# Kernel tuning notes

Measured on AMD Instinct MI355X. Metric: run time of the kernel, lower is better.

Reference implementation:

```python
import jax, jax.numpy as jnp
import numpy as np

H = 64        # index_n_heads
D = 128       # index_head_dim
R = 64        # rope_head_dim
TOPK = 512    # index_topk
FP8_MAX = 448.0
EPS = 1e-6
THETA = 10000.0


def setup_inputs() -> dict:
    key = jax.random.key(0)
    ks = jax.random.split(key, 6)
    T, DM, QL = 1536, 7168, 1536
    return {
        "hidden_states": jax.random.normal(ks[0], (T, DM), jnp.float32),
        "q_lora": jax.random.normal(ks[1], (T, QL), jnp.float32),
        "wq_b": jax.random.normal(ks[2], (QL, H * D), jnp.float32) / np.sqrt(QL),
        "wk": jax.random.normal(ks[3], (DM, D), jnp.float32) / np.sqrt(DM),
        "k_norm_w": jnp.ones((D,), jnp.float32),
        "k_norm_b": jnp.zeros((D,), jnp.float32),
        "weights_proj_w": jax.random.normal(ks[4], (DM, H), jnp.float32) / np.sqrt(DM),
        "positions": jnp.arange(T, dtype=jnp.int32),
    }


def _rope_neox(x, pos):
    # x: [T, ..., R]; pos: [T]. NEOX-style (half-split) rotary on the rope slice.
    half = R // 2
    inv = 1.0 / (THETA ** (jnp.arange(half, dtype=jnp.float32) / half))
    ang = pos.astype(jnp.float32)[:, None] * inv  # [T, half]
    cos, sin = jnp.cos(ang), jnp.sin(ang)
    while cos.ndim < x.ndim:
        cos, sin = cos[:, None, :], sin[:, None, :]
    x1, x2 = x[..., :half], x[..., half:]
    return jnp.concatenate([x1 * cos - x2 * sin, x2 * cos + x1 * sin], axis=-1)


def _fp8_quant(x):
    # per-row (last-dim) e4m3 quantization: value -> fp8 payload + fp32 scale
    scale = jnp.maximum(jnp.max(jnp.abs(x), axis=-1, keepdims=True) / FP8_MAX, 1e-12)
    xq = (x / scale).astype(jnp.float8_e4m3fn).astype(jnp.float32)
    return xq, scale


def reference(hidden_states, q_lora, wq_b, wk, k_norm_w, k_norm_b, weights_proj_w, positions):
    T = hidden_states.shape[0]
    softmax_scale = D ** (-0.5)
    weights_scale = H ** (-0.5)

    # projections
    q = (q_lora @ wq_b).reshape(T, H, D)          # wq_b
    k = hidden_states @ wk                        # wk

    # k_norm (LayerNorm)
    mu = jnp.mean(k, axis=-1, keepdims=True)
    var = jnp.mean((k - mu) ** 2, axis=-1, keepdims=True)
    k = (k - mu) * jax.lax.rsqrt(var + EPS) * k_norm_w + k_norm_b

    # RoPE on the first rope_head_dim dims of q and k
    q = jnp.concatenate([_rope_neox(q[..., :R], positions), q[..., R:]], axis=-1)
    k = jnp.concatenate([_rope_neox(k[..., :R], positions), k[..., R:]], axis=-1)

    # fp8 quantization (per token-head for q, per token for k)
    q_fp8, q_scale = _fp8_quant(q)   # [T,H,D], [T,H,1]
    k_fp8, k_scale = _fp8_quant(k)   # [T,D],   [T,1]

    # head-gate weights: weights_proj(x) * q_scale * softmax_scale * weights_scale
    gate = hidden_states @ weights_proj_w                      # [T,H]
    w = gate[..., None] * q_scale * (softmax_scale * weights_scale)  # [T,H,1]

    # index score: I[t,s] = sum_h w[t,h] * relu(q[t,h] . k[s]) * k_scale[s]
    qk = jnp.einsum('thd,sd->ths', q_fp8, k_fp8)               # [T,H,S]
    score = jnp.einsum('th,ths->ts', w[..., 0], jax.nn.relu(qk))
    score = score * k_scale[:, 0][None, :]

    # causal (ragged prefill) mask + topk block selection
    causal = positions[:, None] >= positions[None, :]
    score = jnp.where(causal, score, -jnp.inf)
    vals, idx = jax.lax.top_k(score, TOPK)
    idx = jnp.where(jnp.isfinite(vals), idx, -1)
    return idx, vals
```

## Files before the change

kernel.cpp:

```cpp
#include <hip/hip_runtime.h>
#include <hip/hip_bf16.h>
#include <math.h>

#define T_SZ 1536
#define DM_SZ 7168
#define QL_SZ 1536
#define H_SZ 64
#define D_SZ 128
#define ND 8192
#define TOPK_SZ 512
#define N2 192
#define SPLITK2 16

typedef float f32x4 __attribute__((ext_vector_type(4)));
typedef short s16x8 __attribute__((ext_vector_type(8)));
typedef unsigned long long u64;

static __device__ __forceinline__ unsigned char f32_to_e4m3(float x){
  unsigned int b = __float_as_uint(x);
  unsigned int s = (b >> 24) & 0x80u;
  float a = fabsf(x);
  if (a < 0.015625f){
    int m = (int)rintf(a * 512.0f);
    if (m == 8) return (unsigned char)(s | 0x08u);
    return (unsigned char)(s | (unsigned)m);
  }
  int e;
  float mant = frexpf(a, &e);
  int E = e - 1;
  int m = (int)rintf(mant * 16.0f) - 8;
  if (m == 8){ E += 1; m = 0; }
  if (E > 8 || (E == 8 && m > 6)) return (unsigned char)(s | 0x7Eu);
  return (unsigned char)(s | ((unsigned)(E + 7) << 3) | (unsigned)m);
}

static __device__ __forceinline__ unsigned short bf16_rne(float x){
  unsigned int u = __float_as_uint(x);
  return (unsigned short)((u + 0x7FFFu + ((u >> 16) & 1u)) >> 16);
}

typedef __attribute__((address_space(1))) const void gas_void;
typedef __attribute__((address_space(3))) void las_void;
static __device__ __forceinline__ void stage16(const void* g, void* l){
  __builtin_amdgcn_global_load_lds((gas_void*)g, (las_void*)l, 16, 0, 0);
}

__global__ void rope_table_k(const int* __restrict__ pos, float* __restrict__ cs){
  int i = blockIdx.x * blockDim.x + threadIdx.x;
  if (i >= T_SZ * 32) return;
  int t = i >> 5, j = i & 31;
  float inv = 1.0f / powf(10000.0f, (float)j * (1.0f / 32.0f));
  float ang = (float)pos[t] * inv;
  cs[t * 64 + j]      = cosf(ang);
  cs[t * 64 + 32 + j] = sinf(ang);
}

__global__ __launch_bounds__(256) void conv_split_k(const float* __restrict__ A,
                                                    unsigned short* __restrict__ hi,
                                                    unsigned short* __restrict__ lo,
                                                    int n4){
  int i = blockIdx.x * 256 + threadIdx.x;
  if (i >= n4) return;
  float4 v = *(const float4*)&A[(size_t)i * 4];
  float f[4] = {v.x, v.y, v.z, v.w};
  unsigned short hb[4], lb[4];
#pragma unroll
  for (int j = 0; j < 4; ++j){
    hb[j] = bf16_rne(f[j]);
    float hf = __uint_as_float((unsigned int)hb[j] << 16);
    lb[j] = bf16_rne(f[j] - hf);
  }
  ushort4 h, l;
  h.x = hb[0]; h.y = hb[1]; h.z = hb[2]; h.w = hb[3];
  l.x = lb[0]; l.y = lb[1]; l.z = lb[2]; l.w = lb[3];
  *(ushort4*)&hi[(size_t)i * 4] = h;
  *(ushort4*)&lo[(size_t)i * 4] = l;
}

__global__ __launch_bounds__(256) void convB_k(const float* __restrict__ B,
                                               unsigned short* __restrict__ bhi,
                                               unsigned short* __restrict__ blo){
  __shared__ float ld[32][33];
  const int n0 = blockIdx.x * 32, k0 = blockIdx.y * 32;
  const int t = threadIdx.x;
  const int r = t >> 3, c4 = (t & 7) * 4;
  float4 v = *(const float4*)&B[(size_t)(k0 + r) * ND + n0 + c4];
  ld[r][c4 + 0] = v.x; ld[r][c4 + 1] = v.y; ld[r][c4 + 2] = v.z; ld[r][c4 + 3] = v.w;
  __syncthreads();
  unsigned short hb[4], lb[4];
#pragma unroll
  for (int j = 0; j < 4; ++j){
    float x = ld[c4 + j][r];
    hb[j] = bf16_rne(x);
    float hf = __uint_as_float((unsigned int)hb[j] << 16);
    lb[j] = bf16_rne(x - hf);
  }
  ushort4 h, l;
  h.x = hb[0]; h.y = hb[1]; h.z = hb[2]; h.w = hb[3];
  l.x = lb[0]; l.y = lb[1]; l.z = lb[2]; l.w = lb[3];
  *(ushort4*)&bhi[(size_t)(n0 + r) * QL_SZ + k0 + c4] = h;
  *(ushort4*)&blo[(size_t)(n0 + r) * QL_SZ + k0 + c4] = l;
}

__global__ __launch_bounds__(256) void conv_w2_k(const float* __restrict__ wk,
                                                 const float* __restrict__ wp,
                                                 unsigned short* __restrict__ bhi,
                                                 unsigned short* __restrict__ blo){
  __shared__ float ld[32][33];
  const int n0 = blockIdx.x * 32, k0 = blockIdx.y * 32;
  const int t = threadIdx.x;
  const int r = t >> 3, c4 = (t & 7) * 4;
  float4 v;
  if (n0 < 128) v = *(const float4*)&wk[(size_t)(k0 + r) * 128 + n0 + c4];
  else          v = *(const float4*)&wp[(size_t)(k0 + r) * 64 + (n0 - 128) + c4];
  ld[r][c4 + 0] = v.x; ld[r][c4 + 1] = v.y; ld[r][c4 + 2] = v.z; ld[r][c4 + 3] = v.w;
  __syncthreads();
  unsigned short hb[4], lb[4];
#pragma unroll
  for (int j = 0; j < 4; ++j){
    float x = ld[c4 + j][r];
    hb[j] = bf16_rne(x);
    float hf = __uint_as_float((unsigned int)hb[j] << 16);
    lb[j] = bf16_rne(x - hf);
  }
  ushort4 h, l;
  h.x = hb[0]; h.y = hb[1]; h.z = hb[2]; h.w = hb[3];
  l.x = lb[0]; l.y = lb[1]; l.z = lb[2]; l.w = lb[3];
  *(ushort4*)&bhi[(size_t)(n0 + r) * DM_SZ + k0 + c4] = h;
  *(ushort4*)&blo[(size_t)(n0 + r) * DM_SZ + k0 + c4] = l;
}

__global__ __launch_bounds__(256) void gemm1_mfma_k(const unsigned short* __restrict__ Ahi,
                                                    const unsigned short* __restrict__ Alo,
                                                    const unsigned short* __restrict__ Bhi,
                                                    const unsigned short* __restrict__ Blo,
                                                    float* __restrict__ C){
  __shared__ unsigned short As [128 * 64];
  __shared__ unsigned short Bs0[128 * 64];
  __shared__ unsigned short Bs1[128 * 64];
  const int bid = blockIdx.x;
  const int lid = (bid & 7) * 96 + (bid >> 3);
  const int mt = lid % 12, nt = lid / 12;
  const int m0 = mt * 128, n0 = nt * 128;
  const int tid = threadIdx.x;
  const int w = tid >> 6, l = tid & 63;
  const int wr = w >> 1, wc = w & 1;
  const int lr = l & 15, lg = l >> 4;

  const int srow = w * 32 + (l >> 3);
  const int ssl  = (l & 7) ^ ((l >> 3) & 7);
  const size_t gA = (size_t)(m0 + srow) * QL_SZ + ssl * 8;
  const size_t gB = (size_t)(n0 + srow) * QL_SZ + ssl * 8;
  const int lbase = w * 2048;

  f32x4 acc[4][4];
#pragma unroll
  for (int i = 0; i < 4; ++i)
#pragma unroll
    for (int j = 0; j < 4; ++j) acc[i][j] = (f32x4){0.f, 0.f, 0.f, 0.f};

  const int amrow = wr * 64 + lr;
  const int bnrow = wc * 64 + lr;

  for (int k0 = 0; k0 < QL_SZ; k0 += 64){
#pragma unroll
    for (int i = 0; i < 4; ++i){
      size_t go = (size_t)i * 8 * QL_SZ + k0;
      stage16(Ahi + gA + go, As  + lbase + i * 512);
      stage16(Bhi + gB + go, Bs0 + lbase + i * 512);
      stage16(Blo + gB + go, Bs1 + lbase + i * 512);
    }
    __syncthreads();
#pragma unroll
    for (int kk = 0; kk < 2; ++kk){
      s16x8 af[4], b0[4], b1[4];
#pragma unroll
      for (int f = 0; f < 4; ++f){
        int ma = amrow + f * 16;
        int nb = bnrow + f * 16;
        int sa = ((kk * 4 + lg) ^ (ma & 7)) * 16;
        int sb = ((kk * 4 + lg) ^ (nb & 7)) * 16;
        af[f] = *(const s16x8*)((const char*)As  + ma * 128 + sa);
        b0[f] = *(const s16x8*)((const char*)Bs0 + nb * 128 + sb);
        b1[f] = *(const s16x8*)((const char*)Bs1 + nb * 128 + sb);
      }
#pragma unroll
      for (int fi = 0; fi < 4; ++fi)
#pragma unroll
        for (int fj = 0; fj < 4; ++fj)
          acc[fi][fj] = __builtin_amdgcn_mfma_f32_16x16x32_bf16(af[fi], b0[fj], acc[fi][fj], 0, 0, 0);
#pragma unroll
      for (int fi = 0; fi < 4; ++fi)
#pragma unroll
        for (int fj = 0; fj < 4; ++fj)
          acc[fi][fj] = __builtin_amdgcn_mfma_f32_16x16x32_bf16(af[fi], b1[fj], acc[fi][fj], 0, 0, 0);
    }
    __syncthreads();
#pragma unroll
    for (int i = 0; i < 4; ++i)
      stage16(Alo + gA + (size_t)i * 8 * QL_SZ + k0, As + lbase + i * 512);
    __syncthreads();
#pragma unroll
    for (int kk = 0; kk < 2; ++kk){
      s16x8 af[4], b0[4];
#pragma unroll
      for (int f = 0; f < 4; ++f){
        int ma = amrow + f * 16;
        int nb = bnrow + f * 16;
        af[f] = *(const s16x8*)((const char*)As  + ma * 128 + (((kk * 4 + lg) ^ (ma & 7)) * 16));
        b0[f] = *(const s16x8*)((const char*)Bs0 + nb * 128 + (((kk * 4 + lg) ^ (nb & 7)) * 16));
      }
#pragma unroll
      for (int fi = 0; fi < 4; ++fi)
#pragma unroll
        for (int fj = 0; fj < 4; ++fj)
          acc[fi][fj] = __builtin_amdgcn_mfma_f32_16x16x32_bf16(af[fi], b0[fj], acc[fi][fj], 0, 0, 0);
    }
    __syncthreads();
  }

#pragma unroll
  for (int fi = 0; fi < 4; ++fi){
    const int row = m0 + wr * 64 + fi * 16 + lg * 4;
#pragma unroll
    for (int fj = 0; fj < 4; ++fj){
      float* cp = C + (size_t)row * ND + n0 + wc * 64 + fj * 16 + lr;
      f32x4 d = acc[fi][fj];
      cp[0]              = d.x;
      cp[(size_t)ND]     = d.y;
      cp[(size_t)2 * ND] = d.z;
      cp[(size_t)3 * ND] = d.w;
    }
  }
}

__global__ __launch_bounds__(128) void gemm2_mfma_k(const unsigned short* __restrict__ Ahi,
                                                    const unsigned short* __restrict__ Alo,
                                                    const unsigned short* __restrict__ Bhi,
                                                    const unsigned short* __restrict__ Blo,
                                                    float* __restrict__ part){
  __shared__ unsigned short As [128 * 64];
  __shared__ unsigned short Bs0[64 * 64];
  __shared__ unsigned short Bs1[64 * 64];
  const int bid = blockIdx.x;
  const int lid = (bid & 7) * 72 + (bid >> 3);
  const int s   = lid / 36;
  const int rem = lid % 36;
  const int mt = rem / 3, nt = rem % 3;
  const int m0 = mt * 128, n0 = nt * 64;
  const int kbeg = s * (DM_SZ / SPLITK2);
  const int tid = threadIdx.x;
  const int w = tid >> 6, l = tid & 63;
  const int lr = l & 15, lg = l >> 4;

  const int srow = tid >> 3;
  const int ssl  = (tid & 7) ^ (srow & 7);
  const size_t gA = (size_t)(m0 + srow) * DM_SZ + ssl * 8;
  const size_t gB = (size_t)(n0 + srow) * DM_SZ + ssl * 8;
  const int lbase = w * 512;

  f32x4 acc[4][4];
#pragma unroll
  for (int i = 0; i < 4; ++i)
#pragma unroll
    for (int j = 0; j < 4; ++j) acc[i][j] = (f32x4){0.f, 0.f, 0.f, 0.f};

  const int amrow = w * 64 + lr;
  const int bnrow = lr;

  for (int k0 = kbeg; k0 < kbeg + DM_SZ / SPLITK2; k0 += 64){
#pragma unroll
    for (int i = 0; i < 8; ++i)
      stage16(Ahi + gA + (size_t)i * 16 * DM_SZ + k0, As + lbase + i * 1024);
#pragma unroll
    for (int i = 0; i < 4; ++i){
      stage16(Bhi + gB + (size_t)i * 16 * DM_SZ + k0, Bs0 + lbase + i * 1024);
      stage16(Blo + gB + (size_t)i * 16 * DM_SZ + k0, Bs1 + lbase + i * 1024);
    }
    __syncthreads();
#pragma unroll
    for (int kk = 0; kk < 2; ++kk){
      s16x8 af[4], b0[4], b1[4];
#pragma unroll
      for (int f = 0; f < 4; ++f){
        int ma = amrow + f * 16;
        int nb = bnrow + f * 16;
        int sa = ((kk * 4 + lg) ^ (ma & 7)) * 16;
        int sb = ((kk * 4 + lg) ^ (nb & 7)) * 16;
        af[f] = *(const s16x8*)((const char*)As  + ma * 128 + sa);
        b0[f] = *(const s16x8*)((const char*)Bs0 + nb * 128 + sb);
        b1[f] = *(const s16x8*)((const char*)Bs1 + nb * 128 + sb);
      }
#pragma unroll
      for (int fi = 0; fi < 4; ++fi)
#pragma unroll
        for (int fj = 0; fj < 4; ++fj)
          acc[fi][fj] = __builtin_amdgcn_mfma_f32_16x16x32_bf16(af[fi], b0[fj], acc[fi][fj], 0, 0, 0);
#pragma unroll
      for (int fi = 0; fi < 4; ++fi)
#pragma unroll
        for (int fj = 0; fj < 4; ++fj)
          acc[fi][fj] = __builtin_amdgcn_mfma_f32_16x16x32_bf16(af[fi], b1[fj], acc[fi][fj], 0, 0, 0);
    }
    __syncthreads();
#pragma unroll
    for (int i = 0; i < 8; ++i)
      stage16(Alo + gA + (size_t)i * 16 * DM_SZ + k0, As + lbase + i * 1024);
    __syncthreads();
#pragma unroll
    for (int kk = 0; kk < 2; ++kk){
      s16x8 af[4], b0[4];
#pragma unroll
      for (int f = 0; f < 4; ++f){
        int ma = amrow + f * 16;
        int nb = bnrow + f * 16;
        af[f] = *(const s16x8*)((const char*)As  + ma * 128 + (((kk * 4 + lg) ^ (ma & 7)) * 16));
        b0[f] = *(const s16x8*)((const char*)Bs0 + nb * 128 + (((kk * 4 + lg) ^ (nb & 7)) * 16));
      }
#pragma unroll
      for (int fi = 0; fi < 4; ++fi)
#pragma unroll
        for (int fj = 0; fj < 4; ++fj)
          acc[fi][fj] = __builtin_amdgcn_mfma_f32_16x16x32_bf16(af[fi], b0[fj], acc[fi][fj], 0, 0, 0);
    }
    __syncthreads();
  }

  float* p = part + (size_t)(s * 36 + mt * 3 + nt) * (128 * 64);
#pragma unroll
  for (int fi = 0; fi < 4; ++fi){
    const int row = w * 64 + fi * 16 + lg * 4;
#pragma unroll
    for (int fj = 0; fj < 4; ++fj){
      float* cp = p + (size_t)row * 64 + fj * 16 + lr;
      f32x4 d = acc[fi][fj];
      cp[  0] = d.x;
      cp[ 64] = d.y;
      cp[128] = d.z;
      cp[192] = d.w;
    }
  }
}

__global__ void gemm2_reduce2_k(const float* __restrict__ part,
                                float* __restrict__ kraw, float* __restrict__ gate){
  int e = blockIdx.x * 256 + threadIdx.x;
  if (e >= T_SZ * N2) return;
  int r = e / N2, c = e % N2;
  int mt = r >> 7, rl = r & 127;
  int nt = c >> 6, cl = c & 63;
  const float* pp = part + (size_t)(mt * 3 + nt) * (128 * 64) + rl * 64 + cl;
  float sum = 0.0f;
#pragma unroll
  for (int s = 0; s < SPLITK2; ++s) sum += pp[(size_t)s * 36 * 128 * 64];
  if (c < 128) kraw[r * 128 + c] = sum;
  else         gate[r * 64 + (c - 128)] = sum;
}

__global__ __launch_bounds__(256) void gemm1_k(const float* __restrict__ A,
                                               const float* __restrict__ B,
                                               float* __restrict__ C){
  __shared__ float As[8][132];
  __shared__ float Bs[8][132];
  const int tid = threadIdx.x;
  const int bm = blockIdx.y * 128, bn = blockIdx.x * 128;
  const int ty = tid >> 4, tx = tid & 15;
  const int arow = tid >> 1, ak = (tid & 1) * 4;
  const int brow = tid >> 5, bcol = (tid & 31) * 4;
  float acc[8][8];
#pragma unroll
  for (int i = 0; i < 8; i++)
#pragma unroll
    for (int j = 0; j < 8; j++) acc[i][j] = 0.0f;

  for (int k0 = 0; k0 < QL_SZ; k0 += 8){
    float4 av = *(const float4*)&A[(size_t)(bm + arow) * QL_SZ + k0 + ak];
    float4 bv = *(const float4*)&B[(size_t)(k0 + brow) * ND + bn + bcol];
    As[ak + 0][arow] = av.x; As[ak + 1][arow] = av.y;
    As[ak + 2][arow] = av.z; As[ak + 3][arow] = av.w;
    *(float4*)&Bs[brow][bcol] = bv;
    __syncthreads();
#pragma unroll
    for (int kk = 0; kk < 8; ++kk){
      float a[8], b[8];
      *(float4*)&a[0] = *(const float4*)&As[kk][ty * 8];
      *(float4*)&a[4] = *(const float4*)&As[kk][ty * 8 + 4];
      *(float4*)&b[0] = *(const float4*)&Bs[kk][tx * 8];
      *(float4*)&b[4] = *(const float4*)&Bs[kk][tx * 8 + 4];
#pragma unroll
      for (int i = 0; i < 8; i++)
#pragma unroll
        for (int j = 0; j < 8; j++) acc[i][j] += a[i] * b[j];
    }
    __syncthreads();
  }
#pragma unroll
  for (int i = 0; i < 8; i++)
#pragma unroll
    for (int j = 0; j < 8; j += 4){
      float4 o; o.x = acc[i][j]; o.y = acc[i][j+1]; o.z = acc[i][j+2]; o.w = acc[i][j+3];
      *(float4*)&C[(size_t)(bm + ty * 8 + i) * ND + bn + tx * 8 + j] = o;
    }
}

__global__ __launch_bounds__(256) void gemm2_partial_k(const float* __restrict__ hs,
                                                       const float* __restrict__ wk,
                                                       const float* __restrict__ wp,
                                                       float* __restrict__ part){
  __shared__ float As[32][33];
  __shared__ float Bs[32][196];
  const int tid = threadIdx.x;
  const int m0 = blockIdx.x * 32;
  const int ks = blockIdx.y;
  const int kbeg = ks * (DM_SZ / 8), kend = kbeg + DM_SZ / 8;
  const int arow = tid >> 3, ak4 = (tid & 7) * 4;
  const int r2 = (tid >> 4) * 2, cg = (tid & 15) * 12;
  float acc[2][12];
#pragma unroll
  for (int i = 0; i < 2; i++)
#pragma unroll
    for (int j = 0; j < 12; j++) acc[i][j] = 0.0f;

  for (int k0 = kbeg; k0 < kend; k0 += 32){
    float4 av = *(const float4*)&hs[(size_t)(m0 + arow) * DM_SZ + k0 + ak4];
    As[ak4 + 0][arow] = av.x; As[ak4 + 1][arow] = av.y;
    As[ak4 + 2][arow] = av.z; As[ak4 + 3][arow] = av.w;
#pragma unroll
    for (int i = 0; i < 6; ++i){
      int fi = tid + i * 256;
      int row = fi / 48, c4 = fi % 48;
      float4 bv;
      if (c4 < 32) bv = *(const float4*)&wk[(size_t)(k0 + row) * 128 + c4 * 4];
      else         bv = *(const float4*)&wp[(size_t)(k0 + row) * 64 + (c4 - 32) * 4];
      *(float4*)&Bs[row][c4 * 4] = bv;
    }
    __syncthreads();
#pragma unroll
    for (int kk = 0; kk < 32; ++kk){
      float a0 = As[kk][r2], a1 = As[kk][r2 + 1];
      float b[12];
      *(float4*)&b[0] = *(const float4*)&Bs[kk][cg];
      *(float4*)&b[4] = *(const float4*)&Bs[kk][cg + 4];
      *(float4*)&b[8] = *(const float4*)&Bs[kk][cg + 8];
#pragma unroll
      for (int j = 0; j < 12; j++){ acc[0][j] += a0 * b[j]; acc[1][j] += a1 * b[j]; }
    }
    __syncthreads();
  }
  float* p = part + (size_t)(ks * 48 + blockIdx.x) * 32 * 192;
#pragma unroll
  for (int i = 0; i < 2; i++)
#pragma unroll
    for (int j = 0; j < 12; j += 4){
      float4 o; o.x = acc[i][j]; o.y = acc[i][j+1]; o.z = acc[i][j+2]; o.w = acc[i][j+3];
      *(float4*)&p[(r2 + i) * 192 + cg + j] = o;
    }
}

__global__ void gemm2_reduce_k(const float* __restrict__ part,
                               float* __restrict__ kraw, float* __restrict__ gate){
  int e = blockIdx.x * 256 + threadIdx.x;
  if (e >= T_SZ * 192) return;
  int r = e / 192, c = e % 192;
  int mt = r >> 5, rl = r & 31;
  float s = 0.0f;
  for (int ks = 0; ks < 8; ++ks)
    s += part[((size_t)(ks * 48 + mt) * 32 + rl) * 192 + c];
  if (c < 128) kraw[r * 128 + c] = s;
  else         gate[r * 64 + (c - 128)] = s;
}

__global__ __launch_bounds__(128) void k_post_k(const float* __restrict__ kraw,
                                                const float* __restrict__ knw,
                                                const float* __restrict__ knb,
                                                const float* __restrict__ cs,
                                                unsigned char* __restrict__ kf8,
                                                float* __restrict__ kscale){
  const int t = blockIdx.x, d = threadIdx.x;
  __shared__ float sh[128];
  __shared__ float red[2];
  float x = kraw[t * 128 + d];
  float v = x;
#pragma unroll
  for (int o = 32; o > 0; o >>= 1) v += __shfl_xor(v, o, 64);
  if ((d & 63) == 0) red[d >> 6] = v;
  __syncthreads();
  float mu = (red[0] + red[1]) / 128.0f;
  float dx = x - mu;
  v = dx * dx;
  __syncthreads();
#pragma unroll
  for (int o = 32; o > 0; o >>= 1) v += __shfl_xor(v, o, 64);
  if ((d & 63) == 0) red[d >> 6] = v;
  __syncthreads();
  float var = (red[0] + red[1]) / 128.0f;
  float nv = dx * (1.0f / sqrtf(var + 1e-6f)) * knw[d] + knb[d];
  sh[d] = nv;
  __syncthreads();
  float outv;
  const float* ct = cs + t * 64;
  if (d < 32)        outv = nv * ct[d] - sh[d + 32] * ct[32 + d];
  else if (d < 64){ int j = d - 32; outv = nv * ct[j] + sh[j] * ct[32 + j]; }
  else               outv = nv;
  v = fabsf(outv);
  __syncthreads();
#pragma unroll
  for (int o = 32; o > 0; o >>= 1) v = fmaxf(v, __shfl_xor(v, o, 64));
  if ((d & 63) == 0) red[d >> 6] = v;
  __syncthreads();
  float amax = fmaxf(red[0], red[1]);
  float scale = fmaxf(amax / 448.0f, 1e-12f);
  kf8[t * 128 + d] = f32_to_e4m3(outv / scale);
  if (d == 0) kscale[t] = scale;
}

__global__ __launch_bounds__(128) void q_post_k(const float* __restrict__ q,
                                                const float* __restrict__ gate,
                                                const float* __restrict__ cs,
                                                unsigned char* __restrict__ qf8,
                                                float* __restrict__ wbuf){
  const int row = blockIdx.x;
  const int d = threadIdx.x;
  const int t = row >> 6;
  __shared__ float sh[128];
  __shared__ float red[2];
  float x = q[(size_t)row * 128 + d];
  sh[d] = x;
  __syncthreads();
  float outv;
  const float* ct = cs + t * 64;
  if (d < 32)        outv = x * ct[d] - sh[d + 32] * ct[32 + d];
  else if (d < 64){ int j = d - 32; outv = x * ct[j] + sh[j] * ct[32 + j]; }
  else               outv = x;
  float v = fabsf(outv);
#pragma unroll
  for (int o = 32; o > 0; o >>= 1) v = fmaxf(v, __shfl_xor(v, o, 64));
  if ((d & 63) == 0) red[d >> 6] = v;
  __syncthreads();
  float amax = fmaxf(red[0], red[1]);
  float scale = fmaxf(amax / 448.0f, 1e-12f);
  qf8[(size_t)row * 128 + d] = f32_to_e4m3(outv / scale);
  if (d == 0) wbuf[row] = gate[row] * scale * 0.011048543456039806f;
}

__global__ __launch_bounds__(256) void score_mfma_k(const unsigned char* __restrict__ qf8,
                                                    const unsigned char* __restrict__ kf8,
                                                    const float* __restrict__ wbuf,
                                                    const float* __restrict__ kscale,
                                                    float* __restrict__ score){
  const int bid = blockIdx.x;
  const int p = bid >> 1;
  const int h0 = (bid & 1) * 32;
  int bt = (int)((sqrtf(8.0f * (float)p + 1.0f) - 1.0f) * 0.5f);
  while ((bt + 1) * (bt + 2) / 2 <= p) ++bt;
  while (bt * (bt + 1) / 2 > p) --bt;
  const int bs = p - bt * (bt + 1) / 2;
  const int t0 = bt * 64, s0 = bs * 64;
  const int tid = threadIdx.x;
  const int w  = tid >> 6;
  const int l  = tid & 63;
  const int lr = l & 15;
  const int lg = l >> 4;

  __shared__ float wl[64][68];
#pragma unroll
  for (int i = 0; i < 4; i++){
    int fi = tid + i * 256;
    int row = fi >> 4, c4 = (fi & 15) * 4;
    *(float4*)&wl[row][c4] = *(const float4*)&wbuf[(t0 + row) * 64 + c4];
  }

  u64 b00,b01,b02,b03, b10,b11,b12,b13, b20,b21,b22,b23, b30,b31,b32,b33;
  {
    const unsigned char* kb = kf8 + (size_t)s0 * 128 + 8 * lg;
    const unsigned char* k0r = kb + (size_t)(lr     ) * 128;
    const unsigned char* k1r = kb + (size_t)(lr + 16) * 128;
    const unsigned char* k2r = kb + (size_t)(lr + 32) * 128;
    const unsigned char* k3r = kb + (size_t)(lr + 48) * 128;
    b00=*(const u64*)(k0r+0);  b01=*(const u64*)(k0r+32); b02=*(const u64*)(k0r+64); b03=*(const u64*)(k0r+96);
    b10=*(const u64*)(k1r+0);  b11=*(const u64*)(k1r+32); b12=*(const u64*)(k1r+64); b13=*(const u64*)(k1r+96);
    b20=*(const u64*)(k2r+0);  b21=*(const u64*)(k2r+32); b22=*(const u64*)(k2r+64); b23=*(const u64*)(k2r+96);
    b30=*(const u64*)(k3r+0);  b31=*(const u64*)(k3r+32); b32=*(const u64*)(k3r+64); b33=*(const u64*)(k3r+96);
  }
  __syncthreads();

  const unsigned char* qp = qf8 + (size_t)(t0 + 16 * w + lr) * 8192 + h0 * 128 + 8 * lg;
  u64 a0 = *(const u64*)(qp +  0), a1 = *(const u64*)(qp + 32),
      a2 = *(const u64*)(qp + 64), a3 = *(const u64*)(qp + 96);

  f32x4 acc0 = {0,0,0,0}, acc1 = {0,0,0,0}, acc2 = {0,0,0,0}, acc3 = {0,0,0,0};
  const int wrow = 16 * w + 4 * lg;

  for (int h = 0; h < 32; ++h){
    const unsigned char* qn = qp + ((h + 1) & 31) * 128;
    u64 p0 = *(const u64*)(qn +  0), p1 = *(const u64*)(qn + 32),
        p2 = *(const u64*)(qn + 64), p3 = *(const u64*)(qn + 96);

    f32x4 c0 = {0,0,0,0}, c1 = {0,0,0,0}, c2 = {0,0,0,0}, c3 = {0,0,0,0};
    c0 = __builtin_amdgcn_mfma_f32_16x16x32_fp8_fp8((long)a0, (long)b00, c0, 0, 0, 0);
    c1 = __builtin_amdgcn_mfma_f32_16x16x32_fp8_fp8((long)a0, (long)b10, c1, 0, 0, 0);
    c2 = __builtin_amdgcn_mfma_f32_16x16x32_fp8_fp8((long)a0, (long)b20, c2, 0, 0, 0);
    c3 = __builtin_amdgcn_mfma_f32_16x16x32_fp8_fp8((long)a0, (long)b30, c3, 0, 0, 0);
    c0 = __builtin_amdgcn_mfma_f32_16x16x32_fp8_fp8((long)a1, (long)b01, c0, 0, 0, 0);
    c1 = __builtin_amdgcn_mfma_f32_16x16x32_fp8_fp8((long)a1, (long)b11, c1, 0, 0, 0);
    c2 = __builtin_amdgcn_mfma_f32_16x16x32_fp8_fp8((long)a1, (long)b21, c2, 0, 0, 0);
    c3 = __builtin_amdgcn_mfma_f32_16x16x32_fp8_fp8((long)a1, (long)b31, c3, 0, 0, 0);
    c0 = __builtin_amdgcn_mfma_f32_16x16x32_fp8_fp8((long)a2, (long)b02, c0, 0, 0, 0);
    c1 = __builtin_amdgcn_mfma_f32_16x16x32_fp8_fp8((long)a2, (long)b12, c1, 0, 0, 0);
    c2 = __builtin_amdgcn_mfma_f32_16x16x32_fp8_fp8((long)a2, (long)b22, c2, 0, 0, 0);
    c3 = __builtin_amdgcn_mfma_f32_16x16x32_fp8_fp8((long)a2, (long)b32, c3, 0, 0, 0);
    c0 = __builtin_amdgcn_mfma_f32_16x16x32_fp8_fp8((long)a3, (long)b03, c0, 0, 0, 0);
    c1 = __builtin_amdgcn_mfma_f32_16x16x32_fp8_fp8((long)a3, (long)b13, c1, 0, 0, 0);
    c2 = __builtin_amdgcn_mfma_f32_16x16x32_fp8_fp8((long)a3, (long)b23, c2, 0, 0, 0);
    c3 = __builtin_amdgcn_mfma_f32_16x16x32_fp8_fp8((long)a3, (long)b33, c3, 0, 0, 0);

    float w0 = wl[wrow + 0][h0 + h], w1 = wl[wrow + 1][h0 + h],
          w2 = wl[wrow + 2][h0 + h], w3 = wl[wrow + 3][h0 + h];
    acc0.x += w0 * fmaxf(c0.x, 0.0f); acc0.y += w1 * fmaxf(c0.y, 0.0f);
    acc0.z += w2 * fmaxf(c0.z, 0.0f); acc0.w += w3 * fmaxf(c0.w, 0.0f);
    acc1.x += w0 * fmaxf(c1.x, 0.0f); acc1.y += w1 * fmaxf(c1.y, 0.0f);
    acc1.z += w2 * fmaxf(c1.z, 0.0f); acc1.w += w3 * fmaxf(c1.w, 0.0f);
    acc2.x += w0 * fmaxf(c2.x, 0.0f); acc2.y += w1 * fmaxf(c2.y, 0.0f);
    acc2.z += w2 * fmaxf(c2.z, 0.0f); acc2.w += w3 * fmaxf(c2.w, 0.0f);
    acc3.x += w0 * fmaxf(c3.x, 0.0f); acc3.y += w1 * fmaxf(c3.y, 0.0f);
    acc3.z += w2 * fmaxf(c3.z, 0.0f); acc3.w += w3 * fmaxf(c3.w, 0.0f);

    a0 = p0; a1 = p1; a2 = p2; a3 = p3;
  }

  const int trow = t0 + 16 * w + 4 * lg;
  float ks0 = kscale[s0 + lr], ks1 = kscale[s0 + 16 + lr],
        ks2 = kscale[s0 + 32 + lr], ks3 = kscale[s0 + 48 + lr];
  float* sbase = score + (size_t)(bid & 1) * T_SZ * T_SZ;
  float* sp0 = sbase + (size_t)(trow + 0) * T_SZ + s0 + lr;
  float* sp1 = sbase + (size_t)(trow + 1) * T_SZ + s0 + lr;
  float* sp2 = sbase + (size_t)(trow + 2) * T_SZ + s0 + lr;
  float* sp3 = sbase + (size_t)(trow + 3) * T_SZ + s0 + lr;
  sp0[ 0] = acc0.x * ks0; sp1[ 0] = acc0.y * ks0; sp2[ 0] = acc0.z * ks0; sp3[ 0] = acc0.w * ks0;
  sp0[16] = acc1.x * ks1; sp1[16] = acc1.y * ks1; sp2[16] = acc1.z * ks1; sp3[16] = acc1.w * ks1;
  sp0[32] = acc2.x * ks2; sp1[32] = acc2.y * ks2; sp2[32] = acc2.z * ks2; sp3[32] = acc2.w * ks2;
  sp0[48] = acc3.x * ks3; sp1[48] = acc3.y * ks3; sp2[48] = acc3.z * ks3; sp3[48] = acc3.w * ks3;
}

__global__ __launch_bounds__(256) void topk_sel_k(const float* __restrict__ score,
                                                  float* __restrict__ out){
  const int t = blockIdx.x, tid = threadIdx.x;
  const int n = t + 1;
  __shared__ unsigned int U[2048];
  __shared__ unsigned long long cand[512];
  __shared__ unsigned int hist[256];
  __shared__ unsigned int tix[1536];
  __shared__ unsigned int cnts[2];
  __shared__ unsigned int sel[2];

  const float* s0row = score + (size_t)t * T_SZ;
  const float* s1row = score + (size_t)T_SZ * T_SZ + (size_t)t * T_SZ;
#pragma unroll
  for (int m = 0; m < 8; ++m){
    int j = tid + m * 256;
    unsigned int u = 0u;
    if (j < n){
      float val = s0row[j] + s1row[j];
      unsigned int b = __float_as_uint(val);
      u = (b & 0x80000000u) ? ~b : (b | 0x80000000u);
    }
    U[j] = u;
  }
  if (tid < 2) cnts[tid] = 0u;
  __syncthreads();

  if (n > 512){
    unsigned int prefix = 0u, rem = 512u;
#pragma unroll
    for (int level = 0; level < 4; ++level){
      const int shift = 24 - 8 * level;
      hist[tid] = 0u;
      __syncthreads();
#pragma unroll
      for (int m = 0; m < 8; ++m){
        unsigned int u = U[tid + m * 256];
        bool match = (u != 0u) && (level == 0 || (u >> (shift + 8)) == prefix);
        if (match) atomicAdd(&hist[(u >> shift) & 255u], 1u);
      }
      __syncthreads();
      if (tid < 64){
        unsigned int c0 = hist[tid*4], c1 = hist[tid*4+1], c2 = hist[tid*4+2], c3 = hist[tid*4+3];
        unsigned int loc = c0 + c1 + c2 + c3;
        unsigned int acc = loc;
        for (int off = 1; off < 64; off <<= 1){
          unsigned int v = __shfl_down(acc, off, 64);
          if (tid + off < 64) acc += v;
        }
        unsigned int S3 = acc - loc;
        unsigned int S2 = S3 + c3;
        unsigned int S1 = S2 + c2;
        unsigned int S0 = S1 + c1;
        if (S0 < rem && rem <= S0 + c0){ sel[0] = tid*4 + 0; sel[1] = S0; }
        if (S1 < rem && rem <= S1 + c1){ sel[0] = tid*4 + 1; sel[1] = S1; }
        if (S2 < rem && rem <= S2 + c2){ sel[0] = tid*4 + 2; sel[1] = S2; }
        if (S3 < rem && rem <= S3 + c3){ sel[0] = tid*4 + 3; sel[1] = S3; }
      }
      __syncthreads();
      prefix = (prefix << 8) | sel[0];
      rem -= sel[1];
    }
    const unsigned int u_thr = prefix;

#pragma unroll
    for (int m = 0; m < 8; ++m){
      int j = tid + m * 256;
      unsigned int u = U[j];
      if (u > u_thr){
        unsigned int p = atomicAdd(&cnts[0], 1u);
        cand[p] = ((unsigned long long)u << 32) | (unsigned int)(~(unsigned int)j);
      } else if (u == u_thr){
        unsigned int q = atomicAdd(&cnts[1], 1u);
        tix[q] = (unsigned int)j;
      }
    }
    __syncthreads();
    const unsigned int G = cnts[0], Tt = cnts[1];
    if (Tt == rem){
      for (unsigned int q = tid; q < Tt; q += 256)
        cand[G + q] = ((unsigned long long)u_thr << 32) | (unsigned int)(~tix[q]);
      __syncthreads();
    } else {
      if (tid < 64) hist[tid] = 0u;
      __syncthreads();
      for (unsigned int q = tid; q < Tt; q += 256) atomicAdd(&hist[tix[q] >> 5], 1u);
      __syncthreads();
      if (tid == 0){
        unsigned int cum = 0; unsigned int d = 0;
        for (; d < 64; ++d){ unsigned int c = hist[d]; if (cum + c >= rem) break; cum += c; }
        sel[0] = d; sel[1] = rem - cum;
      }
      __syncthreads();
      const unsigned int dA = sel[0], remA = sel[1];
      if (tid < 32) hist[64 + tid] = 0u;
      __syncthreads();
      for (unsigned int q = tid; q < Tt; q += 256){
        unsigned int j = tix[q];
        if ((j >> 5) == dA) atomicAdd(&hist[64 + (j & 31u)], 1u);
      }
      __syncthreads();
      if (tid == 0){
        unsigned int cum = 0; unsigned int e = 0;
        for (; e < 32; ++e){ unsigned int c = hist[64 + e]; if (cum + c >= remA) break; cum += c; }
        sel[0] = dA * 32 + e;
        cnts[1] = 0u;
      }
      __syncthreads();
      const unsigned int jthr = sel[0];
      for (unsigned int q = tid; q < Tt; q += 256){
        unsigned int j = tix[q];
        if (j <= jthr){
          unsigned int p = atomicAdd(&cnts[1], 1u);
          cand[G + p] = ((unsigned long long)u_thr << 32) | (unsigned int)(~j);
        }
      }
      __syncthreads();
    }
  } else {
    for (int i = tid; i < 512; i += 256){
      unsigned int u = (i < n) ? U[i] : 0u;
      cand[i] = u ? (((unsigned long long)u << 32) | (unsigned int)(~(unsigned int)i)) : 0ull;
    }
    __syncthreads();
  }

  for (int k = 2; k <= 512; k <<= 1){
    for (int j = k >> 1; j > 0; j >>= 1){
#pragma unroll
      for (int m = 0; m < 2; ++m){
        int i = tid + m * 256;
        int ixj = i ^ j;
        if (ixj > i){
          unsigned long long A = cand[i], B = cand[ixj];
          bool up = (i & k) == 0;
          if (up ? (A < B) : (A > B)){ cand[i] = B; cand[ixj] = A; }
        }
      }
      __syncthreads();
    }
  }

  for (int i = tid; i < TOPK_SZ; i += 256){
    unsigned long long kk = cand[i];
    unsigned int u = (unsigned int)(kk >> 32);
    unsigned int b = (u & 0x80000000u) ? (u & 0x7fffffffu) : ~u;
    float val = __uint_as_float(b);
    int idx = (int)(~(unsigned int)(kk & 0xffffffffu));
    bool fin = (u != 0u) && (val > -__builtin_huge_valf());
    out[(size_t)t * TOPK_SZ + i] = fin ? (float)idx : -1.0f;
    out[(size_t)T_SZ * TOPK_SZ + (size_t)t * TOPK_SZ + i] = fin ? val : -3.0e38f;
  }
}

extern "C" void kernel_launch(void* const* d_in, const int* in_sizes, int n_in,
                              void* d_out, int out_size, void* d_ws, size_t ws_size,
                              hipStream_t stream){
  const float* hs  = (const float*)d_in[0];
  const float* ql  = (const float*)d_in[1];
  const float* wqb = (const float*)d_in[2];
  const float* wk  = (const float*)d_in[3];
  const float* knw = (const float*)d_in[4];
  const float* knb = (const float*)d_in[5];
  const float* wpj = (const float*)d_in[6];
  const int*   pos = (const int*)d_in[7];
  char* ws = (char*)d_ws;
  size_t off = 0;
  auto alloc = [&](size_t b){ size_t o = off; off += (b + 255) & ~(size_t)255; return o; };
  float* cs     = (float*)(ws + alloc((size_t)T_SZ * 64 * 4));
  float* qbuf   = (float*)(ws + alloc((size_t)T_SZ * ND * 4));
  float* kraw   = (float*)(ws + alloc((size_t)T_SZ * 128 * 4));
  float* gate   = (float*)(ws + alloc((size_t)T_SZ * 64 * 4));
  unsigned char* kf8 = (unsigned char*)(ws + alloc((size_t)T_SZ * 128));
  float* kscale = (float*)(ws + alloc((size_t)T_SZ * 4));
  float* wbuf   = (float*)(ws + alloc((size_t)T_SZ * 64 * 4));
  const size_t base2 = off;

  size_t oA = base2;
  auto allocA = [&](size_t b){ size_t o = oA; oA += (b + 255) & ~(size_t)255; return o; };
  unsigned short* hshi = (unsigned short*)(ws + allocA((size_t)T_SZ * DM_SZ * 2));
  unsigned short* hslo = (unsigned short*)(ws + allocA((size_t)T_SZ * DM_SZ * 2));
  unsigned short* w2hi = (unsigned short*)(ws + allocA((size_t)N2 * DM_SZ * 2));
  unsigned short* w2lo = (unsigned short*)(ws + allocA((size_t)N2 * DM_SZ * 2));
  float* part2 = (float*)(ws + allocA((size_t)SPLITK2 * 36 * 128 * 64 * 4));
  const bool fitA = (oA <= ws_size);

  size_t oB = base2;
  auto allocB = [&](size_t b){ size_t o = oB; oB += (b + 255) & ~(size_t)255; return o; };
  unsigned short* Ahi = (unsigned short*)(ws + allocB((size_t)T_SZ * QL_SZ * 2));
  unsigned short* Alo = (unsigned short*)(ws + allocB((size_t)T_SZ * QL_SZ * 2));
  unsigned short* Bth = (unsigned short*)(ws + allocB((size_t)ND * QL_SZ * 2));
  unsigned short* Btl = (unsigned short*)(ws + allocB((size_t)ND * QL_SZ * 2));
  const bool fitB = (oB <= ws_size);

  unsigned char* qf8 = (unsigned char*)(ws + base2);
  float* part_old    = (float*)(ws + base2);
  float* score = qbuf;
  float* out = (float*)d_out;

  rope_table_k<<<dim3((T_SZ * 32 + 255) / 256), dim3(256), 0, stream>>>(pos, cs);

  if (fitA){
    conv_split_k<<<dim3(T_SZ * DM_SZ / 4 / 256), dim3(256), 0, stream>>>(hs, hshi, hslo, T_SZ * DM_SZ / 4);
    conv_w2_k<<<dim3(N2 / 32, DM_SZ / 32), dim3(256), 0, stream>>>(wk, wpj, w2hi, w2lo);
    gemm2_mfma_k<<<dim3(12 * 3 * SPLITK2), dim3(128), 0, stream>>>(hshi, hslo, w2hi, w2lo, part2);
    gemm2_reduce2_k<<<dim3((T_SZ * N2 + 255) / 256), dim3(256), 0, stream>>>(part2, kraw, gate);
  } else {
    gemm2_partial_k<<<dim3(48, 8), dim3(256), 0, stream>>>(hs, wk, wpj, part_old);
    gemm2_reduce_k<<<dim3((T_SZ * 192) / 256), dim3(256), 0, stream>>>(part_old, kraw, gate);
  }
  k_post_k<<<dim3(T_SZ), dim3(128), 0, stream>>>(kraw, knw, knb, cs, kf8, kscale);

  if (fitB){
    conv_split_k<<<dim3(T_SZ * QL_SZ / 4 / 256), dim3(256), 0, stream>>>(ql, Ahi, Alo, T_SZ * QL_SZ / 4);
    convB_k<<<dim3(ND / 32, QL_SZ / 32), dim3(256), 0, stream>>>(wqb, Bth, Btl);
    gemm1_mfma_k<<<dim3(768), dim3(256), 0, stream>>>(Ahi, Alo, Bth, Btl, qbuf);
  } else {
    gemm1_k<<<dim3(ND / 128, T_SZ / 128), dim3(256), 0, stream>>>(ql, wqb, qbuf);
  }
  q_post_k<<<dim3(T_SZ * H_SZ), dim3(128), 0, stream>>>(qbuf, gate, cs, qf8, wbuf);

  score_mfma_k<<<dim3(600), dim3(256), 0, stream>>>(qf8, kf8, wbuf, kscale, score);
  topk_sel_k<<<dim3(T_SZ), dim3(256), 0, stream>>>(score, out);
}
```

Measured before the change: 302.7 us.

## Fuse q RoPE, per-head fp8 quantization and gate weights into gemm1 epilogue

The q-projection GEMM epilogue now applies NEOX RoPE to the rope columns in registers, computes the per-row-per-head absmax with shuffles and shared memory, and writes fp8 q plus the head-gate weights directly. This removes the fp32 qbuf write (1536x8192 floats) and the separate q_post_k pass that read it back. The workspace layout is reshuffled so qf8 and score get dedicated buffers. In exchange, the epilogue gains an extra block barrier, scattered byte stores and more register pressure.

```diff
diff --git a/kernel.cpp b/kernel.cpp
--- a/kernel.cpp
+++ b/kernel.cpp
@@ -134,10 +134,14 @@
                                                     const unsigned short* __restrict__ Alo,
                                                     const unsigned short* __restrict__ Bhi,
                                                     const unsigned short* __restrict__ Blo,
-                                                    float* __restrict__ C){
+                                                    const float* __restrict__ cs,
+                                                    const float* __restrict__ gate,
+                                                    unsigned char* __restrict__ qf8,
+                                                    float* __restrict__ wbuf){
   __shared__ unsigned short As [128 * 64];
   __shared__ unsigned short Bs0[128 * 64];
   __shared__ unsigned short Bs1[128 * 64];
+  __shared__ float amx[2][128];
   const int bid = blockIdx.x;
   const int lid = (bid & 7) * 96 + (bid >> 3);
   const int mt = lid % 12, nt = lid / 12;
@@ -219,17 +223,70 @@
     __syncthreads();
   }
 
+  if (wc == 0){
+#pragma unroll
+    for (int fi = 0; fi < 4; ++fi){
+      const int rbase = m0 + wr * 64 + fi * 16 + lg * 4;
+      float c0a[4], s0a[4], c1a[4], s1a[4];
+#pragma unroll
+      for (int r = 0; r < 4; ++r){
+        const float* ct = cs + (size_t)(rbase + r) * 64;
+        c0a[r] = ct[lr];      s0a[r] = ct[32 + lr];
+        c1a[r] = ct[16 + lr]; s1a[r] = ct[48 + lr];
+      }
+      f32x4 c0 = {c0a[0], c0a[1], c0a[2], c0a[3]};
+      f32x4 s0 = {s0a[0], s0a[1], s0a[2], s0a[3]};
+      f32x4 c1 = {c1a[0], c1a[1], c1a[2], c1a[3]};
+      f32x4 s1 = {s1a[0], s1a[1], s1a[2], s1a[3]};
+      f32x4 x0 = acc[fi][0], x1 = acc[fi][1], x2 = acc[fi][2], x3 = acc[fi][3];
+      acc[fi][0] = x0 * c0 - x2 * s0;
+      acc[fi][1] = x1 * c1 - x3 * s1;
+      acc[fi][2] = x2 * c0 + x0 * s0;
+      acc[fi][3] = x3 * c1 + x1 * s1;
+    }
+  }
 #pragma unroll
   for (int fi = 0; fi < 4; ++fi){
-    const int row = m0 + wr * 64 + fi * 16 + lg * 4;
-#pragma unroll
-    for (int fj = 0; fj < 4; ++fj){
-      float* cp = C + (size_t)row * ND + n0 + wc * 64 + fj * 16 + lr;
-      f32x4 d = acc[fi][fj];
-      cp[0]              = d.x;
-      cp[(size_t)ND]     = d.y;
-      cp[(size_t)2 * ND] = d.z;
-      cp[(size_t)3 * ND] = d.w;
+    float amx4[4];
+    amx4[0] = fmaxf(fmaxf(fabsf(acc[fi][0].x), fabsf(acc[fi][1].x)),
+                    fmaxf(fabsf(acc[fi][2].x), fabsf(acc[fi][3].x)));
+    amx4[1] = fmaxf(fmaxf(fabsf(acc[fi][0].y), fabsf(acc[fi][1].y)),
+                    fmaxf(fabsf(acc[fi][2].y), fabsf(acc[fi][3].y)));
+    amx4[2] = fmaxf(fmaxf(fabsf(acc[fi][0].z), fabsf(acc[fi][1].z)),
+                    fmaxf(fabsf(acc[fi][2].z), fabsf(acc[fi][3].z)));
+    amx4[3] = fmaxf(fmaxf(fabsf(acc[fi][0].w), fabsf(acc[fi][1].w)),
+                    fmaxf(fabsf(acc[fi][2].w), fabsf(acc[fi][3].w)));
+#pragma unroll
+    for (int o = 1; o < 16; o <<= 1){
+#pragma unroll
+      for (int r = 0; r < 4; ++r)
+        amx4[r] = fmaxf(amx4[r], __shfl_xor(amx4[r], o, 64));
+    }
+    if (lr == 0){
+      const int rl = wr * 64 + fi * 16 + lg * 4;
+#pragma unroll
+      for (int r = 0; r < 4; ++r) amx[wc][rl + r] = amx4[r];
+    }
+  }
+  __syncthreads();
+#pragma unroll
+  for (int fi = 0; fi < 4; ++fi){
+    const int rl = wr * 64 + fi * 16 + lg * 4;
+    float v0[4], v1[4], v2[4], v3[4];
+    *(f32x4*)v0 = acc[fi][0]; *(f32x4*)v1 = acc[fi][1];
+    *(f32x4*)v2 = acc[fi][2]; *(f32x4*)v3 = acc[fi][3];
+#pragma unroll
+    for (int r = 0; r < 4; ++r){
+      const int row = m0 + rl + r;
+      float amax = fmaxf(amx[0][rl + r], amx[1][rl + r]);
+      float scale = fmaxf(amax / 448.0f, 1e-12f);
+      unsigned char* qp2 = qf8 + ((size_t)row * 64 + nt) * 128 + wc * 64 + lr;
+      qp2[ 0] = f32_to_e4m3(v0[r] / scale);
+      qp2[16] = f32_to_e4m3(v1[r] / scale);
+      qp2[32] = f32_to_e4m3(v2[r] / scale);
+      qp2[48] = f32_to_e4m3(v3[r] / scale);
+      if (wc == 0 && lr == 0)
+        wbuf[row * 64 + nt] = gate[row * 64 + nt] * scale * 0.011048543456039806f;
     }
   }
 }
@@ -811,12 +868,13 @@
   size_t off = 0;
   auto alloc = [&](size_t b){ size_t o = off; off += (b + 255) & ~(size_t)255; return o; };
   float* cs     = (float*)(ws + alloc((size_t)T_SZ * 64 * 4));
-  float* qbuf   = (float*)(ws + alloc((size_t)T_SZ * ND * 4));
+  float* score  = (float*)(ws + alloc((size_t)2 * T_SZ * T_SZ * 4));
   float* kraw   = (float*)(ws + alloc((size_t)T_SZ * 128 * 4));
   float* gate   = (float*)(ws + alloc((size_t)T_SZ * 64 * 4));
   unsigned char* kf8 = (unsigned char*)(ws + alloc((size_t)T_SZ * 128));
   float* kscale = (float*)(ws + alloc((size_t)T_SZ * 4));
   float* wbuf   = (float*)(ws + alloc((size_t)T_SZ * 64 * 4));
+  unsigned char* qf8 = (unsigned char*)(ws + alloc((size_t)T_SZ * ND));
   const size_t base2 = off;
 
   size_t oA = base2;
@@ -836,9 +894,8 @@
   unsigned short* Btl = (unsigned short*)(ws + allocB((size_t)ND * QL_SZ * 2));
   const bool fitB = (oB <= ws_size);
 
-  unsigned char* qf8 = (unsigned char*)(ws + base2);
-  float* part_old    = (float*)(ws + base2);
-  float* score = qbuf;
+  float* part_old = (float*)(ws + base2);
+  float* qbuf     = (float*)(ws + base2);
   float* out = (float*)d_out;
 
   rope_table_k<<<dim3((T_SZ * 32 + 255) / 256), dim3(256), 0, stream>>>(pos, cs);
@@ -857,11 +914,11 @@
   if (fitB){
     conv_split_k<<<dim3(T_SZ * QL_SZ / 4 / 256), dim3(256), 0, stream>>>(ql, Ahi, Alo, T_SZ * QL_SZ / 4);
     convB_k<<<dim3(ND / 32, QL_SZ / 32), dim3(256), 0, stream>>>(wqb, Bth, Btl);
-    gemm1_mfma_k<<<dim3(768), dim3(256), 0, stream>>>(Ahi, Alo, Bth, Btl, qbuf);
+    gemm1_mfma_k<<<dim3(768), dim3(256), 0, stream>>>(Ahi, Alo, Bth, Btl, cs, gate, qf8, wbuf);
   } else {
     gemm1_k<<<dim3(ND / 128, T_SZ / 128), dim3(256), 0, stream>>>(ql, wqb, qbuf);
-  }
-  q_post_k<<<dim3(T_SZ * H_SZ), dim3(128), 0, stream>>>(qbuf, gate, cs, qf8, wbuf);
+    q_post_k<<<dim3(T_SZ * H_SZ), dim3(128), 0, stream>>>(qbuf, gate, cs, qf8, wbuf);
+  }
 
   score_mfma_k<<<dim3(600), dim3(256), 0, stream>>>(qf8, kf8, wbuf, kscale, score);
   topk_sel_k<<<dim3(T_SZ), dim3(256), 0, stream>>>(score, out);
```

Result: no change. 303.5 us (+0.3%).
